# Performance work log

Measured on AMD Instinct MI355X. Metric: run time of the kernel, lower is better.

The kernel has to match this reference:

```python
import jax, jax.numpy as jnp
import numpy as np

B, S, D = 4, 2048, 1024


def setup_inputs() -> dict:
    key = jax.random.key(0)
    ks = jax.random.split(key, 7)
    s = 1.0 / np.sqrt(D)
    return {
        "x": jax.random.normal(ks[0], (B, S, D), dtype=jnp.float32),
        "Wq": jax.random.normal(ks[1], (D, D), dtype=jnp.float32) * s,
        "bq": jnp.zeros((D,), dtype=jnp.float32),
        "Wk": jax.random.normal(ks[2], (D, D), dtype=jnp.float32) * s,
        "bk": jnp.zeros((D,), dtype=jnp.float32),
        "Wv": jax.random.normal(ks[3], (D, D), dtype=jnp.float32) * s,
        "bv": jnp.zeros((D,), dtype=jnp.float32),
    }


def reference(x, Wq, bq, Wk, bk, Wv, bv):
    # Linear layers: x @ W^T + b (torch nn.Linear convention)
    Q = jnp.einsum("bsd,ed->bse", x, Wq) + bq
    K = jnp.einsum("bsd,ed->bse", x, Wk) + bk
    V = jnp.einsum("bsd,ed->bse", x, Wv) + bv
    scale = 1.0 / (x.shape[-1] ** 0.5)
    scores = jnp.einsum("bse,bte->bst", Q, K) * scale  # [B, S, S]
    attn = jax.nn.softmax(scores, axis=-1)
    out = jnp.einsum("bst,bte->bse", attn, V)
    return out
```

## Files before the change

kernel.cpp:

```cpp
#include <hip/hip_runtime.h>
#include <math.h>


typedef _Float16 f16;
typedef _Float16 f16x8 __attribute__((ext_vector_type(8)));
typedef _Float16 f16x4 __attribute__((ext_vector_type(4)));
typedef float f32x4 __attribute__((ext_vector_type(4)));

__device__ __forceinline__ void glds16(const void* g, const void* l) {
    __builtin_amdgcn_global_load_lds(
        (const __attribute__((address_space(1))) void*)g,
        (__attribute__((address_space(3))) void*)l, 16, 0, 0);
}

#define VMCNT(n)  asm volatile("s_waitcnt vmcnt(" #n ")" ::: "memory")
#define LGKM(n)   asm volatile("s_waitcnt lgkmcnt(" #n ")" ::: "memory")
#define BARRIER() asm volatile("s_barrier" ::: "memory")
#define SCHEDB()  __builtin_amdgcn_sched_barrier(0)

__global__ __launch_bounds__(256) void prep_kernel(
    const float* __restrict__ x,
    const float* __restrict__ Wq, const float* __restrict__ Wk,
    const float* __restrict__ Wv,
    f16* __restrict__ xh, f16* __restrict__ Wh3, float* __restrict__ sums)
{
    const int bid = blockIdx.x, tid = threadIdx.x;
    if (bid < 8) {
        float4 z = {0.f, 0.f, 0.f, 0.f};
        ((float4*)sums)[bid * 256 + tid] = z;
    }
    if (bid < 8192) {
        const int i = bid * 256 + tid;
        float4 v = ((const float4*)x)[i];
        f16x4 h = { (f16)v.x, (f16)v.y, (f16)v.z, (f16)v.w };
        ((f16x4*)xh)[i] = h;
    } else {
        const int wid   = bid - 8192;
        const int plane = wid >> 10;
        const int i     = (wid & 1023) * 256 + tid;
        const float* src = (plane == 0) ? Wq : (plane == 1) ? Wk : Wv;
        float4 v = ((const float4*)src)[i];
        f16x4 h = { (f16)v.x, (f16)v.y, (f16)v.z, (f16)v.w };
        ((f16x4*)(Wh3 + (size_t)plane * 1024 * 1024))[i] = h;
    }
}

#define ABUF 16384
#define BBUF 8192
#define BOFF 49152

__device__ __forceinline__ void mfma_core3(
    const f16* __restrict__ A, int lda,
    const f16* __restrict__ B, int ldb,
    int K, int m0, int n0, f16* sm, f32x4 acc[4][4])
{
    const int tid  = threadIdx.x;
    const int lane = tid & 63;
    const int w    = tid >> 6;
    const int wr   = w >> 1;
    const int wc   = w & 1;
    const int lr   = lane & 15;
    const int kq   = lane >> 4;

    const int rl = lane >> 3;
    const int ch = (lane & 7) ^ rl;

    const f16* gA[4];
    #pragma unroll
    for (int p = 0; p < 4; ++p)
        gA[p] = A + (size_t)(m0 + p * 64 + w * 8 + rl) * lda + ch * 8;
    const f16* gB[2];
    #pragma unroll
    for (int p = 0; p < 2; ++p)
        gB[p] = B + (size_t)(n0 + p * 64 + w * 8 + rl) * ldb + ch * 8;

    const int NT = K >> 6;

    f16* sA0 = sm;             f16* sB0 = sm + BOFF;
    f16* sA1 = sm + ABUF;      f16* sB1 = sm + BOFF + BBUF;
    f16* sA2 = sm + 2 * ABUF;  f16* sB2 = sm + BOFF + 2 * BBUF;

    #define STAGE(kofs, dA, dB) do {                                          \
        _Pragma("unroll")                                                     \
        for (int p = 0; p < 4; ++p)                                           \
            glds16(gA[p] + (kofs), (dA) + w * 512 + p * 4096);                \
        _Pragma("unroll")                                                     \
        for (int p = 0; p < 2; ++p)                                           \
            glds16(gB[p] + (kofs), (dB) + w * 512 + p * 4096);                \
    } while (0)

    STAGE(0,  sA0, sB0);
    STAGE(64, sA1, sB1);

    int kst = 128;
    f16* curA = sA0; f16* curB = sB0;
    f16* nxtA = sA1; f16* nxtB = sB1;
    f16* farA = sA2; f16* farB = sB2;

    for (int t = 0; t < NT; ++t) {
        if (t + 2 < NT) {
            STAGE(kst, farA, farB);
            kst += 64;
            VMCNT(12);
        } else if (t + 1 < NT) {
            VMCNT(6);
        } else {
            VMCNT(0);
        }
        BARRIER();

        #pragma unroll
        for (int kk = 0; kk < 2; ++kk) {
            f16x8 a[4], b[4];
            const int c = kk * 4 + kq;
            #pragma unroll
            for (int i = 0; i < 4; ++i) {
                const int ra = wr * 64 + i * 16 + lr;
                a[i] = *(const f16x8*)&curA[ra * 64 + ((c ^ (ra & 7)) * 8)];
            }
            #pragma unroll
            for (int j = 0; j < 4; ++j) {
                const int rb = wc * 64 + j * 16 + lr;
                b[j] = *(const f16x8*)&curB[rb * 64 + ((c ^ (rb & 7)) * 8)];
            }
            LGKM(0);
            SCHEDB();
            __builtin_amdgcn_s_setprio(1);
            #pragma unroll
            for (int i = 0; i < 4; ++i)
                #pragma unroll
                for (int j = 0; j < 4; ++j)
                    acc[i][j] = __builtin_amdgcn_mfma_f32_16x16x32_f16(a[i], b[j], acc[i][j], 0, 0, 0);
            __builtin_amdgcn_s_setprio(0);
            BARRIER();
        }

        f16* tA = curA; f16* tB = curB;
        curA = nxtA; curB = nxtB;
        nxtA = farA; nxtB = farB;
        farA = tA;   farB = tB;
    }
    #undef STAGE
}

__global__ __launch_bounds__(512) void qkv_mfma_kernel(
    const f16* __restrict__ xh, const f16* __restrict__ Wh,
    const float* __restrict__ bq, const float* __restrict__ bk,
    const float* __restrict__ bv,
    f16* __restrict__ Qh, f16* __restrict__ Kh, f16* __restrict__ Vt)
{
    extern __shared__ __align__(16) f16 smem[];
    int flat = blockIdx.x + 8 * (blockIdx.y + 32 * blockIdx.z);
    flat = (flat & 7) * 96 + (flat >> 3);
    const int bx = flat & 7;
    const int by = (flat >> 3) & 31;
    const int bz = flat >> 8;

    const int m0 = by * 256;
    const int n0 = bx * 128;

    f32x4 acc[4][4];
    #pragma unroll
    for (int i = 0; i < 4; ++i)
        #pragma unroll
        for (int j = 0; j < 4; ++j) acc[i][j] = (f32x4){0.f, 0.f, 0.f, 0.f};

    mfma_core3(xh, 1024, Wh + (size_t)bz * 1024 * 1024, 1024, 1024, m0, n0, smem, acc);

    const int lane = threadIdx.x & 63;
    const int w    = threadIdx.x >> 6;
    const int wm = (w >> 1) * 64;
    const int wn = (w & 1) * 64;
    const int col  = lane & 15;
    const int quad = lane >> 4;

    if (bz == 2) {
        #pragma unroll
        for (int i = 0; i < 4; ++i) {
            const int gmb = m0 + wm + i * 16 + quad * 4;
            const int bb_ = gmb >> 11;
            const int s   = gmb & 2047;
            f16* vtb = Vt + (size_t)bb_ * 1024 * 2048;
            #pragma unroll
            for (int j = 0; j < 4; ++j) {
                const int gn = n0 + wn + j * 16 + col;
                const float bbv = bv[gn];
                f16x4 v = { (f16)(acc[i][j][0] + bbv), (f16)(acc[i][j][1] + bbv),
                            (f16)(acc[i][j][2] + bbv), (f16)(acc[i][j][3] + bbv) };
                *(f16x4*)&vtb[(size_t)gn * 2048 + s] = v;
            }
        }
    } else {
        const float* bias = (bz == 0) ? bq : bk;
        const float  sc   = (bz == 0) ? 0.03125f : 1.0f;
        f16* C = (bz == 0) ? Qh : Kh;
        #pragma unroll
        for (int j = 0; j < 4; ++j) {
            const int gn = n0 + wn + j * 16 + col;
            const float bb = bias[gn];
            #pragma unroll
            for (int i = 0; i < 4; ++i)
                #pragma unroll
                for (int r = 0; r < 4; ++r) {
                    const int gm = m0 + wm + i * 16 + quad * 4 + r;
                    C[(size_t)gm * 1024 + gn] = (f16)((acc[i][j][r] + bb) * sc);
                }
        }
    }
}

__global__ __launch_bounds__(512) void scores_exp_kernel(
    const f16* __restrict__ Qh, const f16* __restrict__ Kh,
    f16* __restrict__ P, float* __restrict__ sums)
{
    extern __shared__ __align__(16) f16 smem[];
    const int b  = blockIdx.z;
    const int m0 = blockIdx.y * 256;
    const int n0 = blockIdx.x * 128;

    f32x4 acc[4][4];
    #pragma unroll
    for (int i = 0; i < 4; ++i)
        #pragma unroll
        for (int j = 0; j < 4; ++j) acc[i][j] = (f32x4){0.f, 0.f, 0.f, 0.f};

    const size_t ao = (size_t)b * 2048 * 1024;
    mfma_core3(Qh + ao, 1024, Kh + ao, 1024, 1024, m0, n0, smem, acc);

    const int lane = threadIdx.x & 63;
    const int w    = threadIdx.x >> 6;
    const int wm = (w >> 1) * 64;
    const int wn = (w & 1) * 64;
    const int col  = lane & 15;
    const int quad = lane >> 4;
    f16* C = P + (size_t)b * 2048 * 2048;

    float rp[4][4];
    #pragma unroll
    for (int i = 0; i < 4; ++i)
        #pragma unroll
        for (int r = 0; r < 4; ++r) rp[i][r] = 0.0f;

    #pragma unroll
    for (int i = 0; i < 4; ++i)
        #pragma unroll
        for (int r = 0; r < 4; ++r) {
            const int gm = m0 + wm + i * 16 + quad * 4 + r;
            #pragma unroll
            for (int j = 0; j < 4; ++j) {
                const int gn = n0 + wn + j * 16 + col;
                const f16 p = (f16)__expf(acc[i][j][r]);
                C[(size_t)gm * 2048 + gn] = p;
                rp[i][r] += (float)p;
            }
        }

    #pragma unroll
    for (int i = 0; i < 4; ++i)
        #pragma unroll
        for (int r = 0; r < 4; ++r) {
            float v = rp[i][r];
            v += __shfl_xor(v, 1);
            v += __shfl_xor(v, 2);
            v += __shfl_xor(v, 4);
            v += __shfl_xor(v, 8);
            rp[i][r] = v;
        }
    if (col == 0) {
        #pragma unroll
        for (int i = 0; i < 4; ++i)
            #pragma unroll
            for (int r = 0; r < 4; ++r) {
                const int row = m0 + wm + i * 16 + quad * 4 + r;
                atomicAdd(&sums[b * 2048 + row], rp[i][r]);
            }
    }
}

__global__ __launch_bounds__(512) void pv_mfma_kernel(
    const f16* __restrict__ P, const f16* __restrict__ Vt,
    const float* __restrict__ sums, float* __restrict__ out)
{
    extern __shared__ __align__(16) f16 smem[];
    const int b  = blockIdx.z;
    const int m0 = blockIdx.y * 256;
    const int n0 = blockIdx.x * 128;

    f32x4 acc[4][4];
    #pragma unroll
    for (int i = 0; i < 4; ++i)
        #pragma unroll
        for (int j = 0; j < 4; ++j) acc[i][j] = (f32x4){0.f, 0.f, 0.f, 0.f};

    const size_t ao = (size_t)b * 2048 * 2048;
    const size_t bo = (size_t)b * 1024 * 2048;
    mfma_core3(P + ao, 2048, Vt + bo, 2048, 2048, m0, n0, smem, acc);

    const int lane = threadIdx.x & 63;
    const int w    = threadIdx.x >> 6;
    const int wm = (w >> 1) * 64;
    const int wn = (w & 1) * 64;
    const int col  = lane & 15;
    const int quad = lane >> 4;
    float* C = out + (size_t)b * 2048 * 1024;

    #pragma unroll
    for (int i = 0; i < 4; ++i)
        #pragma unroll
        for (int r = 0; r < 4; ++r) {
            const int rl = m0 + wm + i * 16 + quad * 4 + r;
            const float inv = 1.0f / sums[b * 2048 + rl];
            #pragma unroll
            for (int j = 0; j < 4; ++j) {
                const int gn = n0 + wn + j * 16 + col;
                C[(size_t)rl * 1024 + gn] = acc[i][j][r] * inv;
            }
        }
}

extern "C" void kernel_launch(void* const* d_in, const int* in_sizes, int n_in,
                              void* d_out, int out_size, void* d_ws, size_t ws_size,
                              hipStream_t stream)
{
    (void)in_sizes; (void)n_in; (void)out_size; (void)ws_size;
    const int Bn = 4, S = 2048, D = 1024;
    const float* x  = (const float*)d_in[0];
    const float* Wq = (const float*)d_in[1];
    const float* bq = (const float*)d_in[2];
    const float* Wk = (const float*)d_in[3];
    const float* bk = (const float*)d_in[4];
    const float* Wv = (const float*)d_in[5];
    const float* bv = (const float*)d_in[6];
    float* out = (float*)d_out;

    const size_t MB = 1024 * 1024;
    char* w = (char*)d_ws;
    f16*   xh   = (f16*)(w + 0 * MB);
    f16*   Wh3  = (f16*)(w + 16 * MB);
    f16*   Qh   = (f16*)(w + 38 * MB);
    f16*   Kh   = (f16*)(w + 54 * MB);
    f16*   Vt   = (f16*)(w + 70 * MB);
    float* sums = (float*)(w + 86 * MB);
    f16*   P    = (f16*)(w + 0 * MB);

    static bool attr_set = false;
    if (!attr_set) {
        (void)hipFuncSetAttribute(reinterpret_cast<const void*>(qkv_mfma_kernel),
                            hipFuncAttributeMaxDynamicSharedMemorySize, 147456);
        (void)hipFuncSetAttribute(reinterpret_cast<const void*>(scores_exp_kernel),
                            hipFuncAttributeMaxDynamicSharedMemorySize, 147456);
        (void)hipFuncSetAttribute(reinterpret_cast<const void*>(pv_mfma_kernel),
                            hipFuncAttributeMaxDynamicSharedMemorySize, 147456);
        attr_set = true;
    }

    prep_kernel<<<dim3(11264), 256, 0, stream>>>(x, Wq, Wk, Wv, xh, Wh3, sums);

    qkv_mfma_kernel<<<dim3(D / 128, (Bn * S) / 256, 3), 512, 147456, stream>>>(
        xh, Wh3, bq, bk, bv, Qh, Kh, Vt);

    scores_exp_kernel<<<dim3(S / 128, S / 256, Bn), 512, 147456, stream>>>(
        Qh, Kh, P, sums);
    pv_mfma_kernel<<<dim3(D / 128, S / 256, Bn), 512, 147456, stream>>>(
        P, Vt, sums, out);
}
```

Before: 260.8 us.

## Fuse all attention stages into one persistent cooperative kernel with grid syncs

Replaces the four separate launches (convert, QKV GEMM, scores+exp, PV GEMM) with a single cooperative kernel of 256 persistent blocks that loops over the tiles of each stage and separates stages with grid-wide syncs. The aim is to remove launch gaps and inter-kernel drain and fill overhead. In exchange it adds grid.sync costs, fixes the grid at one block per CU, and may leave tail imbalance where stage tile counts do not divide evenly. The __restrict__ qualifiers are dropped from buffers whose memory is reused across stages.

```diff
diff --git a/kernel.cpp b/kernel.cpp
--- a/kernel.cpp
+++ b/kernel.cpp
@@ -1,5 +1,8 @@
 #include <hip/hip_runtime.h>
+#include <hip/hip_cooperative_groups.h>
 #include <math.h>
+
+namespace cg = cooperative_groups;
 
 
 typedef _Float16 f16;
@@ -18,40 +21,13 @@
 #define BARRIER() asm volatile("s_barrier" ::: "memory")
 #define SCHEDB()  __builtin_amdgcn_sched_barrier(0)
 
-__global__ __launch_bounds__(256) void prep_kernel(
-    const float* __restrict__ x,
-    const float* __restrict__ Wq, const float* __restrict__ Wk,
-    const float* __restrict__ Wv,
-    f16* __restrict__ xh, f16* __restrict__ Wh3, float* __restrict__ sums)
-{
-    const int bid = blockIdx.x, tid = threadIdx.x;
-    if (bid < 8) {
-        float4 z = {0.f, 0.f, 0.f, 0.f};
-        ((float4*)sums)[bid * 256 + tid] = z;
-    }
-    if (bid < 8192) {
-        const int i = bid * 256 + tid;
-        float4 v = ((const float4*)x)[i];
-        f16x4 h = { (f16)v.x, (f16)v.y, (f16)v.z, (f16)v.w };
-        ((f16x4*)xh)[i] = h;
-    } else {
-        const int wid   = bid - 8192;
-        const int plane = wid >> 10;
-        const int i     = (wid & 1023) * 256 + tid;
-        const float* src = (plane == 0) ? Wq : (plane == 1) ? Wk : Wv;
-        float4 v = ((const float4*)src)[i];
-        f16x4 h = { (f16)v.x, (f16)v.y, (f16)v.z, (f16)v.w };
-        ((f16x4*)(Wh3 + (size_t)plane * 1024 * 1024))[i] = h;
-    }
-}
-
 #define ABUF 16384
 #define BBUF 8192
 #define BOFF 49152
 
 __device__ __forceinline__ void mfma_core3(
-    const f16* __restrict__ A, int lda,
-    const f16* __restrict__ B, int ldb,
+    const f16* A, int lda,
+    const f16* B, int ldb,
     int K, int m0, int n0, f16* sm, f32x4 acc[4][4])
 {
     const int tid  = threadIdx.x;
@@ -143,179 +119,202 @@
     #undef STAGE
 }
 
-__global__ __launch_bounds__(512) void qkv_mfma_kernel(
-    const f16* __restrict__ xh, const f16* __restrict__ Wh,
+__global__ __launch_bounds__(512) void fused_attn_kernel(
+    const float* __restrict__ x,
+    const float* __restrict__ Wq, const float* __restrict__ Wk,
+    const float* __restrict__ Wv,
     const float* __restrict__ bq, const float* __restrict__ bk,
     const float* __restrict__ bv,
-    f16* __restrict__ Qh, f16* __restrict__ Kh, f16* __restrict__ Vt)
+    f16* xh, f16* Wh3, f16* P,
+    f16* __restrict__ Qh, f16* __restrict__ Kh, f16* __restrict__ Vt,
+    float* __restrict__ sums, float* __restrict__ out)
 {
     extern __shared__ __align__(16) f16 smem[];
-    int flat = blockIdx.x + 8 * (blockIdx.y + 32 * blockIdx.z);
-    flat = (flat & 7) * 96 + (flat >> 3);
-    const int bx = flat & 7;
-    const int by = (flat >> 3) & 31;
-    const int bz = flat >> 8;
-
-    const int m0 = by * 256;
-    const int n0 = bx * 128;
-
-    f32x4 acc[4][4];
-    #pragma unroll
-    for (int i = 0; i < 4; ++i)
-        #pragma unroll
-        for (int j = 0; j < 4; ++j) acc[i][j] = (f32x4){0.f, 0.f, 0.f, 0.f};
-
-    mfma_core3(xh, 1024, Wh + (size_t)bz * 1024 * 1024, 1024, 1024, m0, n0, smem, acc);
-
-    const int lane = threadIdx.x & 63;
-    const int w    = threadIdx.x >> 6;
-    const int wm = (w >> 1) * 64;
-    const int wn = (w & 1) * 64;
+    cg::grid_group grid = cg::this_grid();
+
+    const int bid  = blockIdx.x;
+    const int tid  = threadIdx.x;
+    const int lane = tid & 63;
+    const int w    = tid >> 6;
+    const int wm   = (w >> 1) * 64;
+    const int wn   = (w & 1) * 64;
     const int col  = lane & 15;
     const int quad = lane >> 4;
 
-    if (bz == 2) {
-        #pragma unroll
-        for (int i = 0; i < 4; ++i) {
-            const int gmb = m0 + wm + i * 16 + quad * 4;
-            const int bb_ = gmb >> 11;
-            const int s   = gmb & 2047;
-            f16* vtb = Vt + (size_t)bb_ * 1024 * 2048;
+    {
+        const int gt = bid * 512 + tid;
+        if (gt < 2048) {
+            float4 z = {0.f, 0.f, 0.f, 0.f};
+            ((float4*)sums)[gt] = z;
+        }
+        #pragma unroll 2
+        for (int k = 0; k < 16; ++k) {
+            const int i = k * 131072 + gt;
+            float4 v = ((const float4*)x)[i];
+            f16x4 h = { (f16)v.x, (f16)v.y, (f16)v.z, (f16)v.w };
+            ((f16x4*)xh)[i] = h;
+        }
+        #pragma unroll
+        for (int p = 0; p < 3; ++p) {
+            const float* src = (p == 0) ? Wq : (p == 1) ? Wk : Wv;
+            f16* dst = Wh3 + (size_t)p * 1048576;
+            #pragma unroll
+            for (int k = 0; k < 2; ++k) {
+                const int i = k * 131072 + gt;
+                float4 v = ((const float4*)src)[i];
+                f16x4 h = { (f16)v.x, (f16)v.y, (f16)v.z, (f16)v.w };
+                ((f16x4*)dst)[i] = h;
+            }
+        }
+    }
+    grid.sync();
+
+    for (int rr = 0; rr < 3; ++rr) {
+        const int t = bid + rr * 256;
+        const int flat = (t & 7) * 96 + (t >> 3);
+        const int bx = flat & 7;
+        const int by = (flat >> 3) & 31;
+        const int bz = flat >> 8;
+        const int m0 = by * 256;
+        const int n0 = bx * 128;
+
+        f32x4 acc[4][4];
+        #pragma unroll
+        for (int i = 0; i < 4; ++i)
+            #pragma unroll
+            for (int j = 0; j < 4; ++j) acc[i][j] = (f32x4){0.f, 0.f, 0.f, 0.f};
+
+        mfma_core3(xh, 1024, Wh3 + (size_t)bz * 1048576, 1024, 1024, m0, n0, smem, acc);
+
+        if (bz == 2) {
+            #pragma unroll
+            for (int i = 0; i < 4; ++i) {
+                const int gmb = m0 + wm + i * 16 + quad * 4;
+                const int bb_ = gmb >> 11;
+                const int s   = gmb & 2047;
+                f16* vtb = Vt + (size_t)bb_ * 1024 * 2048;
+                #pragma unroll
+                for (int j = 0; j < 4; ++j) {
+                    const int gn = n0 + wn + j * 16 + col;
+                    const float bbv = bv[gn];
+                    f16x4 v = { (f16)(acc[i][j][0] + bbv), (f16)(acc[i][j][1] + bbv),
+                                (f16)(acc[i][j][2] + bbv), (f16)(acc[i][j][3] + bbv) };
+                    *(f16x4*)&vtb[(size_t)gn * 2048 + s] = v;
+                }
+            }
+        } else {
+            const float* bias = (bz == 0) ? bq : bk;
+            const float  sc   = (bz == 0) ? 0.03125f : 1.0f;
+            f16* C = (bz == 0) ? Qh : Kh;
             #pragma unroll
             for (int j = 0; j < 4; ++j) {
                 const int gn = n0 + wn + j * 16 + col;
-                const float bbv = bv[gn];
-                f16x4 v = { (f16)(acc[i][j][0] + bbv), (f16)(acc[i][j][1] + bbv),
-                            (f16)(acc[i][j][2] + bbv), (f16)(acc[i][j][3] + bbv) };
-                *(f16x4*)&vtb[(size_t)gn * 2048 + s] = v;
-            }
-        }
-    } else {
-        const float* bias = (bz == 0) ? bq : bk;
-        const float  sc   = (bz == 0) ? 0.03125f : 1.0f;
-        f16* C = (bz == 0) ? Qh : Kh;
-        #pragma unroll
-        for (int j = 0; j < 4; ++j) {
-            const int gn = n0 + wn + j * 16 + col;
-            const float bb = bias[gn];
+                const float bb = bias[gn];
+                #pragma unroll
+                for (int i = 0; i < 4; ++i)
+                    #pragma unroll
+                    for (int r = 0; r < 4; ++r) {
+                        const int gm = m0 + wm + i * 16 + quad * 4 + r;
+                        C[(size_t)gm * 1024 + gn] = (f16)((acc[i][j][r] + bb) * sc);
+                    }
+            }
+        }
+    }
+    grid.sync();
+
+    for (int rr = 0; rr < 2; ++rr) {
+        const int t = bid + rr * 256;
+        const int bx = t & 15;
+        const int by = (t >> 4) & 7;
+        const int b  = t >> 7;
+        const int m0 = by * 256;
+        const int n0 = bx * 128;
+
+        f32x4 acc[4][4];
+        #pragma unroll
+        for (int i = 0; i < 4; ++i)
+            #pragma unroll
+            for (int j = 0; j < 4; ++j) acc[i][j] = (f32x4){0.f, 0.f, 0.f, 0.f};
+
+        const size_t ao = (size_t)b * 2048 * 1024;
+        mfma_core3(Qh + ao, 1024, Kh + ao, 1024, 1024, m0, n0, smem, acc);
+
+        f16* C = P + (size_t)b * 2048 * 2048;
+        float rp[4][4];
+        #pragma unroll
+        for (int i = 0; i < 4; ++i)
+            #pragma unroll
+            for (int r = 0; r < 4; ++r) rp[i][r] = 0.0f;
+
+        #pragma unroll
+        for (int i = 0; i < 4; ++i)
+            #pragma unroll
+            for (int r = 0; r < 4; ++r) {
+                const int gm = m0 + wm + i * 16 + quad * 4 + r;
+                #pragma unroll
+                for (int j = 0; j < 4; ++j) {
+                    const int gn = n0 + wn + j * 16 + col;
+                    const f16 p = (f16)__expf(acc[i][j][r]);
+                    C[(size_t)gm * 2048 + gn] = p;
+                    rp[i][r] += (float)p;
+                }
+            }
+
+        #pragma unroll
+        for (int i = 0; i < 4; ++i)
+            #pragma unroll
+            for (int r = 0; r < 4; ++r) {
+                float v = rp[i][r];
+                v += __shfl_xor(v, 1);
+                v += __shfl_xor(v, 2);
+                v += __shfl_xor(v, 4);
+                v += __shfl_xor(v, 8);
+                rp[i][r] = v;
+            }
+        if (col == 0) {
             #pragma unroll
             for (int i = 0; i < 4; ++i)
                 #pragma unroll
                 for (int r = 0; r < 4; ++r) {
-                    const int gm = m0 + wm + i * 16 + quad * 4 + r;
-                    C[(size_t)gm * 1024 + gn] = (f16)((acc[i][j][r] + bb) * sc);
+                    const int row = m0 + wm + i * 16 + quad * 4 + r;
+                    atomicAdd(&sums[b * 2048 + row], rp[i][r]);
                 }
         }
     }
-}
-
-__global__ __launch_bounds__(512) void scores_exp_kernel(
-    const f16* __restrict__ Qh, const f16* __restrict__ Kh,
-    f16* __restrict__ P, float* __restrict__ sums)
-{
-    extern __shared__ __align__(16) f16 smem[];
-    const int b  = blockIdx.z;
-    const int m0 = blockIdx.y * 256;
-    const int n0 = blockIdx.x * 128;
-
-    f32x4 acc[4][4];
-    #pragma unroll
-    for (int i = 0; i < 4; ++i)
-        #pragma unroll
-        for (int j = 0; j < 4; ++j) acc[i][j] = (f32x4){0.f, 0.f, 0.f, 0.f};
-
-    const size_t ao = (size_t)b * 2048 * 1024;
-    mfma_core3(Qh + ao, 1024, Kh + ao, 1024, 1024, m0, n0, smem, acc);
-
-    const int lane = threadIdx.x & 63;
-    const int w    = threadIdx.x >> 6;
-    const int wm = (w >> 1) * 64;
-    const int wn = (w & 1) * 64;
-    const int col  = lane & 15;
-    const int quad = lane >> 4;
-    f16* C = P + (size_t)b * 2048 * 2048;
-
-    float rp[4][4];
-    #pragma unroll
-    for (int i = 0; i < 4; ++i)
-        #pragma unroll
-        for (int r = 0; r < 4; ++r) rp[i][r] = 0.0f;
-
-    #pragma unroll
-    for (int i = 0; i < 4; ++i)
-        #pragma unroll
-        for (int r = 0; r < 4; ++r) {
-            const int gm = m0 + wm + i * 16 + quad * 4 + r;
-            #pragma unroll
-            for (int j = 0; j < 4; ++j) {
-                const int gn = n0 + wn + j * 16 + col;
-                const f16 p = (f16)__expf(acc[i][j][r]);
-                C[(size_t)gm * 2048 + gn] = p;
-                rp[i][r] += (float)p;
-            }
-        }
-
-    #pragma unroll
-    for (int i = 0; i < 4; ++i)
-        #pragma unroll
-        for (int r = 0; r < 4; ++r) {
-            float v = rp[i][r];
-            v += __shfl_xor(v, 1);
-            v += __shfl_xor(v, 2);
-            v += __shfl_xor(v, 4);
-            v += __shfl_xor(v, 8);
-            rp[i][r] = v;
-        }
-    if (col == 0) {
+    grid.sync();
+
+    {
+        const int t  = bid;
+        const int bx = t & 7;
+        const int by = (t >> 3) & 7;
+        const int b  = t >> 6;
+        const int m0 = by * 256;
+        const int n0 = bx * 128;
+
+        f32x4 acc[4][4];
+        #pragma unroll
+        for (int i = 0; i < 4; ++i)
+            #pragma unroll
+            for (int j = 0; j < 4; ++j) acc[i][j] = (f32x4){0.f, 0.f, 0.f, 0.f};
+
+        const size_t ao = (size_t)b * 2048 * 2048;
+        const size_t bo = (size_t)b * 1024 * 2048;
+        mfma_core3(P + ao, 2048, Vt + bo, 2048, 2048, m0, n0, smem, acc);
+
+        float* C = out + (size_t)b * 2048 * 1024;
         #pragma unroll
         for (int i = 0; i < 4; ++i)
             #pragma unroll
             for (int r = 0; r < 4; ++r) {
-                const int row = m0 + wm + i * 16 + quad * 4 + r;
-                atomicAdd(&sums[b * 2048 + row], rp[i][r]);
-            }
-    }
-}
-
-__global__ __launch_bounds__(512) void pv_mfma_kernel(
-    const f16* __restrict__ P, const f16* __restrict__ Vt,
-    const float* __restrict__ sums, float* __restrict__ out)
-{
-    extern __shared__ __align__(16) f16 smem[];
-    const int b  = blockIdx.z;
-    const int m0 = blockIdx.y * 256;
-    const int n0 = blockIdx.x * 128;
-
-    f32x4 acc[4][4];
-    #pragma unroll
-    for (int i = 0; i < 4; ++i)
-        #pragma unroll
-        for (int j = 0; j < 4; ++j) acc[i][j] = (f32x4){0.f, 0.f, 0.f, 0.f};
-
-    const size_t ao = (size_t)b * 2048 * 2048;
-    const size_t bo = (size_t)b * 1024 * 2048;
-    mfma_core3(P + ao, 2048, Vt + bo, 2048, 2048, m0, n0, smem, acc);
-
-    const int lane = threadIdx.x & 63;
-    const int w    = threadIdx.x >> 6;
-    const int wm = (w >> 1) * 64;
-    const int wn = (w & 1) * 64;
-    const int col  = lane & 15;
-    const int quad = lane >> 4;
-    float* C = out + (size_t)b * 2048 * 1024;
-
-    #pragma unroll
-    for (int i = 0; i < 4; ++i)
-        #pragma unroll
-        for (int r = 0; r < 4; ++r) {
-            const int rl = m0 + wm + i * 16 + quad * 4 + r;
-            const float inv = 1.0f / sums[b * 2048 + rl];
-            #pragma unroll
-            for (int j = 0; j < 4; ++j) {
-                const int gn = n0 + wn + j * 16 + col;
-                C[(size_t)rl * 1024 + gn] = acc[i][j][r] * inv;
-            }
-        }
+                const int rl = m0 + wm + i * 16 + quad * 4 + r;
+                const float inv = 1.0f / sums[b * 2048 + rl];
+                #pragma unroll
+                for (int j = 0; j < 4; ++j) {
+                    const int gn = n0 + wn + j * 16 + col;
+                    C[(size_t)rl * 1024 + gn] = acc[i][j][r] * inv;
+                }
+            }
+    }
 }
 
 extern "C" void kernel_launch(void* const* d_in, const int* in_sizes, int n_in,
@@ -323,7 +322,6 @@
                               hipStream_t stream)
 {
     (void)in_sizes; (void)n_in; (void)out_size; (void)ws_size;
-    const int Bn = 4, S = 2048, D = 1024;
     const float* x  = (const float*)d_in[0];
     const float* Wq = (const float*)d_in[1];
     const float* bq = (const float*)d_in[2];
@@ -345,22 +343,19 @@
 
     static bool attr_set = false;
     if (!attr_set) {
-        (void)hipFuncSetAttribute(reinterpret_cast<const void*>(qkv_mfma_kernel),
-                            hipFuncAttributeMaxDynamicSharedMemorySize, 147456);
-        (void)hipFuncSetAttribute(reinterpret_cast<const void*>(scores_exp_kernel),
-                            hipFuncAttributeMaxDynamicSharedMemorySize, 147456);
-        (void)hipFuncSetAttribute(reinterpret_cast<const void*>(pv_mfma_kernel),
+        (void)hipFuncSetAttribute(reinterpret_cast<const void*>(fused_attn_kernel),
                             hipFuncAttributeMaxDynamicSharedMemorySize, 147456);
         attr_set = true;
     }
 
-    prep_kernel<<<dim3(11264), 256, 0, stream>>>(x, Wq, Wk, Wv, xh, Wh3, sums);
-
-    qkv_mfma_kernel<<<dim3(D / 128, (Bn * S) / 256, 3), 512, 147456, stream>>>(
-        xh, Wh3, bq, bk, bv, Qh, Kh, Vt);
-
-    scores_exp_kernel<<<dim3(S / 128, S / 256, Bn), 512, 147456, stream>>>(
-        Qh, Kh, P, sums);
-    pv_mfma_kernel<<<dim3(D / 128, S / 256, Bn), 512, 147456, stream>>>(
-        P, Vt, sums, out);
+    void* args[] = {
+        (void*)&x, (void*)&Wq, (void*)&Wk, (void*)&Wv,
+        (void*)&bq, (void*)&bk, (void*)&bv,
+        (void*)&xh, (void*)&Wh3, (void*)&P,
+        (void*)&Qh, (void*)&Kh, (void*)&Vt,
+        (void*)&sums, (void*)&out
+    };
+    (void)hipLaunchCooperativeKernel(
+        reinterpret_cast<void*>(fused_attn_kernel),
+        dim3(256), dim3(512), args, 147456, stream);
 }
```

Result: slower. 364.3 us (+39.7%).

## Use 256x256 tiles with double-buffered core for scores kernel

Applied to the files above, without the earlier changes.

Adds a new MFMA mainloop in which each wave computes a 128x64 sub-tile (8x4 MFMA tiles), so the block covers 256x256 of the output, with two-stage LDS buffering instead of three. The scores/exp kernel switches to it, halving the grid along N and raising per-block reuse of the Q and K tiles loaded into LDS. The shared core also drops the barrier between its two k-substeps, and restrict qualifiers are removed. The larger accumulator set raises register pressure, and the launch bound of two blocks per CU may not hold with 128KB of LDS per block.

```diff
diff --git a/kernel.cpp b/kernel.cpp
--- a/kernel.cpp
+++ b/kernel.cpp
@@ -50,8 +50,8 @@
 #define BOFF 49152
 
 __device__ __forceinline__ void mfma_core3(
-    const f16* __restrict__ A, int lda,
-    const f16* __restrict__ B, int ldb,
+    const f16* A, int lda,
+    const f16* B, int ldb,
     int K, int m0, int n0, f16* sm, f32x4 acc[4][4])
 {
     const int tid  = threadIdx.x;
@@ -109,19 +109,17 @@
         }
         BARRIER();
 
-        #pragma unroll
-        for (int kk = 0; kk < 2; ++kk) {
+        {
             f16x8 a[4], b[4];
-            const int c = kk * 4 + kq;
             #pragma unroll
             for (int i = 0; i < 4; ++i) {
                 const int ra = wr * 64 + i * 16 + lr;
-                a[i] = *(const f16x8*)&curA[ra * 64 + ((c ^ (ra & 7)) * 8)];
+                a[i] = *(const f16x8*)&curA[ra * 64 + ((kq ^ (ra & 7)) * 8)];
             }
             #pragma unroll
             for (int j = 0; j < 4; ++j) {
                 const int rb = wc * 64 + j * 16 + lr;
-                b[j] = *(const f16x8*)&curB[rb * 64 + ((c ^ (rb & 7)) * 8)];
+                b[j] = *(const f16x8*)&curB[rb * 64 + ((kq ^ (rb & 7)) * 8)];
             }
             LGKM(0);
             SCHEDB();
@@ -132,7 +130,30 @@
                 for (int j = 0; j < 4; ++j)
                     acc[i][j] = __builtin_amdgcn_mfma_f32_16x16x32_f16(a[i], b[j], acc[i][j], 0, 0, 0);
             __builtin_amdgcn_s_setprio(0);
+        }
+        {
+            f16x8 a[4], b[4];
+            const int c = 4 + kq;
+            #pragma unroll
+            for (int i = 0; i < 4; ++i) {
+                const int ra = wr * 64 + i * 16 + lr;
+                a[i] = *(const f16x8*)&curA[ra * 64 + ((c ^ (ra & 7)) * 8)];
+            }
+            #pragma unroll
+            for (int j = 0; j < 4; ++j) {
+                const int rb = wc * 64 + j * 16 + lr;
+                b[j] = *(const f16x8*)&curB[rb * 64 + ((c ^ (rb & 7)) * 8)];
+            }
+            LGKM(0);
             BARRIER();
+            SCHEDB();
+            __builtin_amdgcn_s_setprio(1);
+            #pragma unroll
+            for (int i = 0; i < 4; ++i)
+                #pragma unroll
+                for (int j = 0; j < 4; ++j)
+                    acc[i][j] = __builtin_amdgcn_mfma_f32_16x16x32_f16(a[i], b[j], acc[i][j], 0, 0, 0);
+            __builtin_amdgcn_s_setprio(0);
         }
 
         f16* tA = curA; f16* tB = curB;
@@ -141,6 +162,92 @@
         farA = tA;   farB = tB;
     }
     #undef STAGE
+}
+
+__device__ __forceinline__ void mfma_core8w(
+    const f16* A, int lda,
+    const f16* B, int ldb,
+    int K, int m0, int n0, f16* sm, f32x4 (&acc)[8][4])
+{
+    const int tid  = threadIdx.x;
+    const int lane = tid & 63;
+    const int w    = tid >> 6;
+    const int wr   = w >> 2;
+    const int wn   = w & 3;
+    const int lr   = lane & 15;
+    const int kq   = lane >> 4;
+
+    const int rl = lane >> 3;
+    const int ch = (lane & 7) ^ rl;
+
+    const f16* gA[4];
+    #pragma unroll
+    for (int p = 0; p < 4; ++p)
+        gA[p] = A + (size_t)(m0 + p * 64 + w * 8 + rl) * lda + ch * 8;
+    const f16* gB[4];
+    #pragma unroll
+    for (int p = 0; p < 4; ++p)
+        gB[p] = B + (size_t)(n0 + p * 64 + w * 8 + rl) * ldb + ch * 8;
+
+    const int NT = K >> 6;
+
+    f16* sA0 = sm;              f16* sA1 = sm + 16384;
+    f16* sB0 = sm + 32768;      f16* sB1 = sm + 49152;
+
+    #define STAGE8(kofs, dA, dB) do {                                         \
+        _Pragma("unroll")                                                     \
+        for (int p = 0; p < 4; ++p)                                           \
+            glds16(gA[p] + (kofs), (dA) + w * 512 + p * 4096);                \
+        _Pragma("unroll")                                                     \
+        for (int p = 0; p < 4; ++p)                                           \
+            glds16(gB[p] + (kofs), (dB) + w * 512 + p * 4096);                \
+    } while (0)
+
+    STAGE8(0, sA0, sB0);
+
+    f16* curA = sA0; f16* curB = sB0;
+    f16* othA = sA1; f16* othB = sB1;
+
+    for (int t = 0; t < NT; ++t) {
+        if (t + 1 < NT) {
+            STAGE8((t + 1) * 64, othA, othB);
+            VMCNT(8);
+        } else {
+            VMCNT(0);
+        }
+        BARRIER();
+
+        #pragma unroll
+        for (int kk = 0; kk < 2; ++kk) {
+            f16x8 a[8], b[4];
+            const int c = kk * 4 + kq;
+            #pragma unroll
+            for (int i = 0; i < 8; ++i) {
+                const int ra = wr * 128 + i * 16 + lr;
+                a[i] = *(const f16x8*)&curA[ra * 64 + ((c ^ (ra & 7)) * 8)];
+            }
+            #pragma unroll
+            for (int j = 0; j < 4; ++j) {
+                const int rb = wn * 64 + j * 16 + lr;
+                b[j] = *(const f16x8*)&curB[rb * 64 + ((c ^ (rb & 7)) * 8)];
+            }
+            LGKM(0);
+            if (kk == 1) BARRIER();
+            SCHEDB();
+            __builtin_amdgcn_s_setprio(1);
+            #pragma unroll
+            for (int i = 0; i < 8; ++i)
+                #pragma unroll
+                for (int j = 0; j < 4; ++j)
+                    acc[i][j] = __builtin_amdgcn_mfma_f32_16x16x32_f16(a[i], b[j], acc[i][j], 0, 0, 0);
+            __builtin_amdgcn_s_setprio(0);
+        }
+
+        f16* x;
+        x = curA; curA = othA; othA = x;
+        x = curB; curB = othB; othB = x;
+    }
+    #undef STAGE8
 }
 
 __global__ __launch_bounds__(512) void qkv_mfma_kernel(
@@ -209,46 +316,45 @@
     }
 }
 
-__global__ __launch_bounds__(512) void scores_exp_kernel(
+__global__ __launch_bounds__(512, 2) void scores_exp_kernel(
     const f16* __restrict__ Qh, const f16* __restrict__ Kh,
     f16* __restrict__ P, float* __restrict__ sums)
 {
     extern __shared__ __align__(16) f16 smem[];
     const int b  = blockIdx.z;
     const int m0 = blockIdx.y * 256;
-    const int n0 = blockIdx.x * 128;
-
-    f32x4 acc[4][4];
-    #pragma unroll
-    for (int i = 0; i < 4; ++i)
+    const int n0 = blockIdx.x * 256;
+
+    f32x4 acc[8][4];
+    #pragma unroll
+    for (int i = 0; i < 8; ++i)
         #pragma unroll
         for (int j = 0; j < 4; ++j) acc[i][j] = (f32x4){0.f, 0.f, 0.f, 0.f};
 
     const size_t ao = (size_t)b * 2048 * 1024;
-    mfma_core3(Qh + ao, 1024, Kh + ao, 1024, 1024, m0, n0, smem, acc);
+    mfma_core8w(Qh + ao, 1024, Kh + ao, 1024, 1024, m0, n0, smem, acc);
 
     const int lane = threadIdx.x & 63;
     const int w    = threadIdx.x >> 6;
-    const int wm = (w >> 1) * 64;
-    const int wn = (w & 1) * 64;
+    const int wr = w >> 2, wn = w & 3;
     const int col  = lane & 15;
     const int quad = lane >> 4;
     f16* C = P + (size_t)b * 2048 * 2048;
 
-    float rp[4][4];
-    #pragma unroll
-    for (int i = 0; i < 4; ++i)
+    float rp[8][4];
+    #pragma unroll
+    for (int i = 0; i < 8; ++i)
         #pragma unroll
         for (int r = 0; r < 4; ++r) rp[i][r] = 0.0f;
 
     #pragma unroll
-    for (int i = 0; i < 4; ++i)
+    for (int i = 0; i < 8; ++i)
         #pragma unroll
         for (int r = 0; r < 4; ++r) {
-            const int gm = m0 + wm + i * 16 + quad * 4 + r;
-            #pragma unroll
-            for (int j = 0; j < 4; ++j) {
-                const int gn = n0 + wn + j * 16 + col;
+            const int gm = m0 + wr * 128 + i * 16 + quad * 4 + r;
+            #pragma unroll
+            for (int j = 0; j < 4; ++j) {
+                const int gn = n0 + wn * 64 + j * 16 + col;
                 const f16 p = (f16)__expf(acc[i][j][r]);
                 C[(size_t)gm * 2048 + gn] = p;
                 rp[i][r] += (float)p;
@@ -256,7 +362,7 @@
         }
 
     #pragma unroll
-    for (int i = 0; i < 4; ++i)
+    for (int i = 0; i < 8; ++i)
         #pragma unroll
         for (int r = 0; r < 4; ++r) {
             float v = rp[i][r];
@@ -268,10 +374,10 @@
         }
     if (col == 0) {
         #pragma unroll
-        for (int i = 0; i < 4; ++i)
+        for (int i = 0; i < 8; ++i)
             #pragma unroll
             for (int r = 0; r < 4; ++r) {
-                const int row = m0 + wm + i * 16 + quad * 4 + r;
+                const int row = m0 + wr * 128 + i * 16 + quad * 4 + r;
                 atomicAdd(&sums[b * 2048 + row], rp[i][r]);
             }
     }
@@ -348,7 +454,7 @@
         (void)hipFuncSetAttribute(reinterpret_cast<const void*>(qkv_mfma_kernel),
                             hipFuncAttributeMaxDynamicSharedMemorySize, 147456);
         (void)hipFuncSetAttribute(reinterpret_cast<const void*>(scores_exp_kernel),
-                            hipFuncAttributeMaxDynamicSharedMemorySize, 147456);
+                            hipFuncAttributeMaxDynamicSharedMemorySize, 131072);
         (void)hipFuncSetAttribute(reinterpret_cast<const void*>(pv_mfma_kernel),
                             hipFuncAttributeMaxDynamicSharedMemorySize, 147456);
         attr_set = true;
@@ -359,7 +465,7 @@
     qkv_mfma_kernel<<<dim3(D / 128, (Bn * S) / 256, 3), 512, 147456, stream>>>(
         xh, Wh3, bq, bk, bv, Qh, Kh, Vt);
 
-    scores_exp_kernel<<<dim3(S / 128, S / 256, Bn), 512, 147456, stream>>>(
+    scores_exp_kernel<<<dim3(S / 256, S / 256, Bn), 512, 131072, stream>>>(
         Qh, Kh, P, sums);
     pv_mfma_kernel<<<dim3(D / 128, S / 256, Bn), 512, 147456, stream>>>(
         P, Vt, sums, out);
```

Result: faster. 247.4 us (-5.1%).
